# Optimization experiments

Hardware: AMD Instinct MI355X
Metric: run time of the kernel (lower is better)

The kernel has to match this reference:

```python
import jax, jax.numpy as jnp
import numpy as np
from jax import lax

P, T, A = 4096, 128, 32
K = int(P * 0.1)          # elite count = 409
TEMP, MOM, MIN_STD = 0.5, 0.1, 0.05
INF = jnp.float32(1e30)   # large finite stand-in for +inf (grad-safe)


def setup_inputs() -> dict:
    key = jax.random.key(0)
    k1, k2 = jax.random.split(key)
    obs_diffs = jax.random.uniform(k1, (P, T, T), dtype=jnp.float32)  # pairwise MSE costs >= 0
    means = jnp.zeros((T, 1, A), dtype=jnp.float32)
    stds = jnp.ones((T, 1, A), dtype=jnp.float32)
    noise = jax.random.normal(k2, (T, P, A), dtype=jnp.float32)
    return {"obs_diffs": obs_diffs, "means": means, "stds": stds, "noise": noise}


def _dtw_dists(obs_diffs):
    """DTW-style min-plus DP: D[i+1,j+1] = min(D[i,j+1], D[i+1,j], D[i,j]) + c[i,j].
    obs_diffs: [P, T, T] -> dists: [P] (= D[:, T, T])."""
    p = obs_diffs.shape[0]
    inf_col = jnp.full((p,), INF, dtype=obs_diffs.dtype)
    # row 0 of the (T+1)x(T+1) table: [0, inf, inf, ...]
    row0 = jnp.concatenate([jnp.zeros((p, 1), obs_diffs.dtype),
                            jnp.full((p, obs_diffs.shape[1]), INF, obs_diffs.dtype)], axis=1)

    def row_step(prev_row, c_row):  # prev_row [P, T+1], c_row [P, T]
        def inner(carry, xs):        # carry = new[j] (left neighbor), vectorized over P
            p_j1, p_j, c = xs        # prev[j+1], prev[j], cost  -- each [P]
            new = jnp.minimum(jnp.minimum(p_j1, p_j), carry) + c
            return new, new
        xs = (prev_row[:, 1:].T, prev_row[:, :-1].T, c_row.T)  # each [T, P]
        _, vals = lax.scan(inner, inf_col, xs)                  # vals [T, P]
        new_row = jnp.concatenate([inf_col[:, None], vals.T], axis=1)
        return new_row, None

    final_row, _ = lax.scan(row_step, row0, jnp.swapaxes(obs_diffs, 0, 1))
    return final_row[:, -1]


def reference(obs_diffs, means, stds, noise):
    # sample population of action trajectories
    actions = jnp.clip(means + stds * noise, -1.0, 1.0)        # [T, P, A]
    dists = _dtw_dists(obs_diffs)                               # [P]
    neg_top, idxs = lax.top_k(-dists, K)                        # K smallest dists
    elite_diffs = -neg_top                                      # [K]
    elite_actions = actions[:, idxs]                            # [T, K, A]
    min_diff = elite_diffs.min()
    score = jnp.exp(TEMP * (min_diff - elite_diffs))
    score = score / score.sum()
    ssum = score.sum()                                          # == 1, kept to match torch
    w = score[None, :, None]                                    # [1, K, 1]
    _mean = jnp.sum(w * elite_actions, axis=1, keepdims=True) / (ssum + 1e-9)   # [T,1,A]
    _std = jnp.sqrt(jnp.sum(w * (elite_actions - _mean) ** 2, axis=1, keepdims=True) / (ssum + 1e-9))
    _std = jnp.clip(_std, MIN_STD, 1.0)
    means_new = MOM * means + (1.0 - MOM) * _mean
    return jnp.stack([means_new, _std])                         # [2, T, 1, A]
```

## Files before the change

kernel.cpp:

```cpp
#include <hip/hip_runtime.h>
#include <math.h>

#define P_N 4096
#define T_N 128
#define A_N 32
#define K_N 409
#define TEMP_C 0.5f
#define MOM_C 0.1f
#define MIN_STD_C 0.05f
#define INF_F 1e30f

__global__ __launch_bounds__(256) void dtw_kernel(const float* __restrict__ obs,
                                                  float* __restrict__ dists) {
  const int tid  = threadIdx.x;
  const int wave = tid >> 6;
  const int lane = tid & 63;
  const int half = lane >> 5;
  const int l    = lane & 31;
  const int p    = blockIdx.x * 8 + wave * 2 + half;

  const float4* row = (const float4*)(obs + (size_t)p * (T_N * T_N)) + l;

  float P1 = INF_F, P2 = INF_F, P3 = INF_F, P4 = INF_F;
  float p0 = (l == 0) ? 0.0f : INF_F;

  float4 cb0 = row[0];
  float4 cb1 = row[32];

  for (int r = 0; r < T_N; ++r) {
    float4 c = cb0;
    cb0 = cb1;
    int rn = r + 2; if (rn > T_N - 1) rn = T_N - 1;
    cb1 = row[rn * 32];

    float a1 = fminf(P1, p0);
    float a2 = fminf(P2, P1);
    float a3 = fminf(P3, P2);
    float a4 = fminf(P4, P3);

    float B = a1 + c.x;
    float C = c.x;
    B = fminf(B + c.y, a2 + c.y); C += c.y;
    B = fminf(B + c.z, a3 + c.z); C += c.z;
    B = fminf(B + c.w, a4 + c.w); C += c.w;

    #pragma unroll
    for (int d = 1; d < 32; d <<= 1) {
      float Bp = __shfl_up(B, (unsigned)d, 32);
      float Cp = __shfl_up(C, (unsigned)d, 32);
      if (l >= d) { B = fminf(Bp + C, B); C = Cp + C; }
    }

    float x = __shfl_up(B, 1u, 32);
    if (l == 0) x = INF_F;

    float n1 = fminf(a1, x)  + c.x;
    float n2 = fminf(a2, n1) + c.y;
    float n3 = fminf(a3, n2) + c.z;
    float n4 = fminf(a4, n3) + c.w;

    p0 = x; P1 = n1; P2 = n2; P3 = n3; P4 = n4;
  }

  if (l == 31) dists[p] = P4;
}

__global__ __launch_bounds__(1024) void select_kernel(const float* __restrict__ dists,
                                                      int* __restrict__ elite_idx,
                                                      float* __restrict__ elite_wn,
                                                      float* __restrict__ meta) {
  __shared__ unsigned int skey[P_N];
  __shared__ unsigned int hist[256];
  __shared__ float elite_d[K_N];
  __shared__ int eqbuf[256];
  __shared__ float red[1024];
  __shared__ unsigned int sc_prefix, sc_minkey;
  __shared__ int sc_r, sc_cntlt, sc_cnteq;

  const int tid = threadIdx.x;

  unsigned int localmin = 0xFFFFFFFFu;
  for (int p = tid; p < P_N; p += 1024) {
    unsigned int k = __float_as_uint(dists[p]);
    skey[p] = k;
    if (k < localmin) localmin = k;
  }
  #pragma unroll
  for (int d = 32; d > 0; d >>= 1) {
    unsigned int o = __shfl_xor(localmin, (unsigned)d, 64);
    if (o < localmin) localmin = o;
  }
  if (tid == 0) { sc_minkey = 0xFFFFFFFFu; sc_cntlt = 0; sc_cnteq = 0;
                  sc_prefix = 0; sc_r = K_N - 1; }
  __syncthreads();
  if ((tid & 63) == 0) atomicMin(&sc_minkey, localmin);
  __syncthreads();

  unsigned int mask = 0;
  for (int shift = 24; shift >= 0; shift -= 8) {
    for (int b = tid; b < 256; b += 1024) hist[b] = 0;
    __syncthreads();
    unsigned int pref = sc_prefix;
    for (int p = tid; p < P_N; p += 1024) {
      unsigned int k = skey[p];
      if ((k & mask) == pref) atomicAdd(&hist[(k >> shift) & 255u], 1u);
    }
    __syncthreads();
    if (tid == 0) {
      int r = sc_r;
      unsigned int cum = 0;
      int bsel = 255;
      for (int b = 0; b < 256; ++b) {
        unsigned int h = hist[b];
        if ((unsigned int)r < cum + h) { bsel = b; break; }
        cum += h;
      }
      sc_prefix |= ((unsigned int)bsel) << shift;
      sc_r = r - (int)cum;
    }
    mask |= 0xFFu << shift;
    __syncthreads();
  }

  const unsigned int tk = sc_prefix;
  const int needeq = sc_r + 1;

  for (int p = tid; p < P_N; p += 1024) {
    unsigned int k = skey[p];
    if (k < tk) {
      int pos = atomicAdd(&sc_cntlt, 1);
      elite_idx[pos] = p;
      elite_d[pos]   = __uint_as_float(k);
    } else if (k == tk) {
      int ep = atomicAdd(&sc_cnteq, 1);
      if (ep < 256) eqbuf[ep] = p;
    }
  }
  __syncthreads();
  if (tid == 0) {
    int cl = sc_cntlt;
    int ce = sc_cnteq; if (ce > 256) ce = 256;
    for (int rsel = 0; rsel < needeq; ++rsel) {
      int best = 0x7FFFFFFF, bi = 0;
      for (int m = 0; m < ce; ++m) {
        int v = eqbuf[m];
        if (v < best) { best = v; bi = m; }
      }
      eqbuf[bi] = 0x7FFFFFFF;
      elite_idx[cl + rsel] = best;
      elite_d[cl + rsel]   = __uint_as_float(tk);
    }
  }
  __syncthreads();

  const float minf = __uint_as_float(sc_minkey);
  float s = 0.0f;
  if (tid < K_N) s = expf(TEMP_C * (minf - elite_d[tid]));
  red[tid] = s;
  for (int d = 512; d > 0; d >>= 1) {
    __syncthreads();
    if (tid < d) red[tid] += red[tid + d];
  }
  __syncthreads();
  const float S = red[0];
  __syncthreads();
  const float wn = (tid < K_N) ? (s / S) : 0.0f;
  red[tid] = wn;
  for (int d = 512; d > 0; d >>= 1) {
    __syncthreads();
    if (tid < d) red[tid] += red[tid + d];
  }
  __syncthreads();
  if (tid < K_N) elite_wn[tid] = wn;
  if (tid == 0) meta[0] = red[0];
}

__global__ __launch_bounds__(256) void elite_stats_kernel(
    const float* __restrict__ noise, const float* __restrict__ means,
    const float* __restrict__ stds, const int* __restrict__ elite_idx,
    const float* __restrict__ elite_wn, const float* __restrict__ meta,
    float* __restrict__ out) {
  const int t = blockIdx.x;
  const int tid = threadIdx.x;
  const int a  = tid & 31;
  const int er = tid >> 5;
  __shared__ int   sidx[K_N];
  __shared__ float swn[K_N];
  __shared__ float sM[8][32];
  __shared__ float sQ[8][32];

  for (int e = tid; e < K_N; e += 256) { sidx[e] = elite_idx[e]; swn[e] = elite_wn[e]; }
  __syncthreads();

  const float mn = means[t * A_N + a];
  const float sd = stds[t * A_N + a];
  const float* nrow = noise + (size_t)t * P_N * A_N;

  float M = 0.0f, Q = 0.0f;
  for (int e = er; e < K_N; e += 8) {
    const int idx = sidx[e];
    const float w = swn[e];
    float x = mn + sd * nrow[idx * A_N + a];
    x = fminf(1.0f, fmaxf(-1.0f, x));
    M += w * x;
    Q += w * x * x;
  }
  sM[er][a] = M; sQ[er][a] = Q;
  __syncthreads();

  if (tid < 32) {
    float Ms = 0.0f, Qs = 0.0f;
    #pragma unroll
    for (int r = 0; r < 8; ++r) { Ms += sM[r][a]; Qs += sQ[r][a]; }
    const float ssum = meta[0];
    const float D = ssum + 1e-9f;
    const float mu = Ms / D;
    float var = (Qs - 2.0f * mu * Ms + mu * mu * ssum) / D;
    float stdv = sqrtf(fmaxf(var, 0.0f));
    stdv = fminf(1.0f, fmaxf(MIN_STD_C, stdv));
    out[t * A_N + a]              = MOM_C * mn + (1.0f - MOM_C) * mu;
    out[T_N * A_N + t * A_N + a]  = stdv;
  }
}

extern "C" void kernel_launch(void* const* d_in, const int* in_sizes, int n_in,
                              void* d_out, int out_size, void* d_ws, size_t ws_size,
                              hipStream_t stream) {
  const float* obs   = (const float*)d_in[0];
  const float* means = (const float*)d_in[1];
  const float* stds  = (const float*)d_in[2];
  const float* noise = (const float*)d_in[3];
  float* out = (float*)d_out;

  float* dists     = (float*)d_ws;
  int*   elite_idx = (int*)(dists + P_N);
  float* elite_wn  = (float*)(elite_idx + 512);
  float* meta      = elite_wn + 512;

  dtw_kernel<<<P_N / 8, 256, 0, stream>>>(obs, dists);
  select_kernel<<<1, 1024, 0, stream>>>(dists, elite_idx, elite_wn, meta);
  elite_stats_kernel<<<T_N, 256, 0, stream>>>(noise, means, stds,
                                              elite_idx, elite_wn, meta, out);
}
```

Measured before the change: 465.6 us.

## Use DPP row shifts for DTW scan and parallelize radix-select bucket search

Replaces the shuffle-based prefix scan in the DTW kernel with DPP row_shr and row_bcast moves that pass identity values in directly, removing the per-step lane predicates. It also computes the cost sum C once outside the scan and deepens the row prefetch from two rows to three. In the select kernel, the serial single-thread bucket search over the 256-entry histogram becomes a 64-lane wave prefix scan. The DPP control codes assume a specific 32-lane row and bank layout, which adds a correctness risk if the bcast semantics differ from what the code expects.

```diff
diff --git a/kernel.cpp b/kernel.cpp
--- a/kernel.cpp
+++ b/kernel.cpp
@@ -10,6 +10,14 @@
 #define MIN_STD_C 0.05f
 #define INF_F 1e30f
 
+#define DPPMOV(dst, src, ctrl, oldv)                                          \
+  {                                                                           \
+    union { float f; int i; } _a, _b, _r;                                     \
+    _a.f = (src); _b.f = (oldv);                                              \
+    _r.i = __builtin_amdgcn_update_dpp(_b.i, _a.i, (ctrl), 0xF, 0xF, false);  \
+    (dst) = _r.f;                                                             \
+  }
+
 __global__ __launch_bounds__(256) void dtw_kernel(const float* __restrict__ obs,
                                                   float* __restrict__ dists) {
   const int tid  = threadIdx.x;
@@ -18,20 +26,22 @@
   const int half = lane >> 5;
   const int l    = lane & 31;
   const int p    = blockIdx.x * 8 + wave * 2 + half;
+  const bool is0 = (l == 0);
 
   const float4* row = (const float4*)(obs + (size_t)p * (T_N * T_N)) + l;
 
   float P1 = INF_F, P2 = INF_F, P3 = INF_F, P4 = INF_F;
-  float p0 = (l == 0) ? 0.0f : INF_F;
+  float p0 = is0 ? 0.0f : INF_F;
 
   float4 cb0 = row[0];
   float4 cb1 = row[32];
+  float4 cb2 = row[64];
 
   for (int r = 0; r < T_N; ++r) {
     float4 c = cb0;
-    cb0 = cb1;
-    int rn = r + 2; if (rn > T_N - 1) rn = T_N - 1;
-    cb1 = row[rn * 32];
+    cb0 = cb1; cb1 = cb2;
+    int rn = r + 3; if (rn > T_N - 1) rn = T_N - 1;
+    cb2 = row[rn * 32];
 
     float a1 = fminf(P1, p0);
     float a2 = fminf(P2, P1);
@@ -39,20 +49,26 @@
     float a4 = fminf(P4, P3);
 
     float B = a1 + c.x;
-    float C = c.x;
-    B = fminf(B + c.y, a2 + c.y); C += c.y;
-    B = fminf(B + c.z, a3 + c.z); C += c.z;
-    B = fminf(B + c.w, a4 + c.w); C += c.w;
-
-    #pragma unroll
-    for (int d = 1; d < 32; d <<= 1) {
-      float Bp = __shfl_up(B, (unsigned)d, 32);
-      float Cp = __shfl_up(C, (unsigned)d, 32);
-      if (l >= d) { B = fminf(Bp + C, B); C = Cp + C; }
-    }
-
-    float x = __shfl_up(B, 1u, 32);
-    if (l == 0) x = INF_F;
+    B = fminf(B + c.y, a2 + c.y);
+    B = fminf(B + c.z, a3 + c.z);
+    B = fminf(B + c.w, a4 + c.w);
+    float C = (c.x + c.y) + (c.z + c.w);
+
+    float Bp, Cp;
+    DPPMOV(Bp, B, 0x111, INF_F); DPPMOV(Cp, C, 0x111, 0.0f);
+    B = fminf(Bp + C, B); C = Cp + C;
+    DPPMOV(Bp, B, 0x112, INF_F); DPPMOV(Cp, C, 0x112, 0.0f);
+    B = fminf(Bp + C, B); C = Cp + C;
+    DPPMOV(Bp, B, 0x114, INF_F); DPPMOV(Cp, C, 0x114, 0.0f);
+    B = fminf(Bp + C, B); C = Cp + C;
+    DPPMOV(Bp, B, 0x118, INF_F); DPPMOV(Cp, C, 0x118, 0.0f);
+    B = fminf(Bp + C, B); C = Cp + C;
+    DPPMOV(Bp, B, 0x142, INF_F); DPPMOV(Cp, C, 0x142, 0.0f);
+    B = fminf(Bp + C, B); C = Cp + C;
+
+    float x;
+    DPPMOV(x, B, 0x138, INF_F);
+    x = is0 ? INF_F : x;
 
     float n1 = fminf(a1, x)  + c.x;
     float n2 = fminf(a2, n1) + c.y;
@@ -70,7 +86,7 @@
                                                       float* __restrict__ elite_wn,
                                                       float* __restrict__ meta) {
   __shared__ unsigned int skey[P_N];
-  __shared__ unsigned int hist[256];
+  __shared__ __align__(16) unsigned int hist[256];
   __shared__ float elite_d[K_N];
   __shared__ int eqbuf[256];
   __shared__ float red[1024];
@@ -106,17 +122,27 @@
       if ((k & mask) == pref) atomicAdd(&hist[(k >> shift) & 255u], 1u);
     }
     __syncthreads();
-    if (tid == 0) {
-      int r = sc_r;
-      unsigned int cum = 0;
-      int bsel = 255;
-      for (int b = 0; b < 256; ++b) {
-        unsigned int h = hist[b];
-        if ((unsigned int)r < cum + h) { bsel = b; break; }
-        cum += h;
+    if (tid < 64) {
+      unsigned h0 = hist[tid * 4 + 0], h1 = hist[tid * 4 + 1];
+      unsigned h2 = hist[tid * 4 + 2], h3 = hist[tid * 4 + 3];
+      unsigned s1 = h0 + h1, s2 = s1 + h2, s3 = s2 + h3;
+      unsigned tot = s3;
+      #pragma unroll
+      for (int d = 1; d < 64; d <<= 1) {
+        unsigned o = __shfl_up(tot, (unsigned)d, 64);
+        if (tid >= d) tot += o;
       }
-      sc_prefix |= ((unsigned int)bsel) << shift;
-      sc_r = r - (int)cum;
+      unsigned base = tot - s3;
+      unsigned rr = (unsigned)sc_r;
+      if (rr >= base && rr < base + s3) {
+        int bsel; unsigned lo;
+        if (rr < base + h0)      { bsel = 0; lo = base; }
+        else if (rr < base + s1) { bsel = 1; lo = base + h0; }
+        else if (rr < base + s2) { bsel = 2; lo = base + s1; }
+        else                     { bsel = 3; lo = base + s2; }
+        sc_prefix |= (unsigned)(tid * 4 + bsel) << shift;
+        sc_r = (int)(rr - lo);
+      }
     }
     mask |= 0xFFu << shift;
     __syncthreads();
```

Result: faster. 448.3 us (-3.7%).
